# Kernel optimization log

Measured on AMD Instinct MI355X. Metric: run time of the kernel, lower is better.

## Reference

```python
import jax, jax.numpy as jnp
import numpy as np

N_NODES = 50000
D_IN = 128
D_OUT = 128
N_EDGES = 800000


def setup_inputs() -> dict:
    key = jax.random.key(0)
    ks = jax.random.split(key, 6)
    x = jax.random.normal(ks[0], (N_NODES, D_IN), dtype=jnp.float32)
    # xavier-uniform-ish init for the per-support weights
    limit = float(np.sqrt(6.0 / (D_IN + D_OUT)))
    weights = jax.random.uniform(ks[1], (2, D_IN, D_OUT), dtype=jnp.float32,
                                 minval=-limit, maxval=limit)
    edge_idx0 = jax.random.randint(ks[2], (2, N_EDGES), 0, N_NODES, dtype=jnp.int64 if jax.config.jax_enable_x64 else jnp.int32)
    vals0 = jax.random.uniform(ks[3], (N_EDGES,), dtype=jnp.float32)
    edge_idx1 = jax.random.randint(ks[4], (2, N_EDGES), 0, N_NODES, dtype=jnp.int64 if jax.config.jax_enable_x64 else jnp.int32)
    vals1 = jax.random.uniform(ks[5], (N_EDGES,), dtype=jnp.float32)
    return {"x": x, "weights": weights, "edge_idx0": edge_idx0, "vals0": vals0,
            "edge_idx1": edge_idx1, "vals1": vals1}


def _spmm(edge_idx, vals, dense, n_rows):
    # (sparse COO A) @ dense : out[row] += vals * dense[col]
    rows, cols = edge_idx[0], edge_idx[1]
    gathered = dense[cols] * vals[:, None]  # [E, D_OUT]
    return jax.ops.segment_sum(gathered, rows, num_segments=n_rows)


def reference(x, weights, edge_idx0, vals0, edge_idx1, vals1):
    n = x.shape[0]
    out = jnp.zeros((n, D_OUT), dtype=x.dtype)
    for w, ei, v in ((weights[0], edge_idx0, vals0), (weights[1], edge_idx1, vals1)):
        pre_sup = x @ w                       # [N, D_OUT] dense GEMM
        out = out + _spmm(ei, v, pre_sup, n)  # SpMM accumulate
    return jax.nn.relu(out)
```

## Files before the change

kernel.cpp:

```cpp
#include <hip/hip_runtime.h>

#define N_NODES 50000
#define D 128
#define N_EDGES 800000
#define SCAN_BLOCKS ((N_NODES + 255) / 256)
#define GEMM_BLOCKS ((N_NODES + 63) / 64)
#define BINS 196
#define NB1 256
#define CH1 3125
#define P2_CAP 9472

typedef __attribute__((ext_vector_type(8))) short short8;
typedef __attribute__((ext_vector_type(4))) float f32x4;

__device__ __forceinline__ unsigned short f2bf(float f) {
    unsigned u = __builtin_bit_cast(unsigned, f);
    u += 0x7FFFu + ((u >> 16) & 1u);
    return (unsigned short)(u >> 16);
}
__device__ __forceinline__ float bflo(unsigned p) {
    return __builtin_bit_cast(float, p << 16);
}
__device__ __forceinline__ float bfhi(unsigned p) {
    return __builtin_bit_cast(float, p & 0xFFFF0000u);
}

__global__ __launch_bounds__(256) void wt_build(const float* __restrict__ w,
                                                unsigned short* __restrict__ wt) {
    int i = blockIdx.x * 256 + threadIdx.x;
    if (i < 2 * D * D) {
        int s = i >> 14, rem = i & 16383, c = rem >> 7, k = rem & 127;
        wt[i] = f2bf(w[s * D * D + k * D + c]);
    }
}

template<int NS>
__device__ __forceinline__ void gemm_body(const float* __restrict__ x,
                                          const unsigned short* __restrict__ wt,
                                          unsigned short* __restrict__ pre0,
                                          unsigned short* __restrict__ pre1,
                                          int n_rows, int blk) {
    const int lane = threadIdx.x & 63;
    const int wid  = threadIdx.x >> 6;
    const int q    = lane >> 4;
    const int rlo  = lane & 15;
    const int r0   = blk * 64 + wid * 16;
    if (r0 >= n_rows) return;

    const float4* x4 = (const float4*)x;
    int arow  = r0 + rlo;
    int arowc = arow < n_rows ? arow : n_rows - 1;

    short8 afr[4];
    #pragma unroll
    for (int kb = 0; kb < 4; ++kb) {
        float4 fa = x4[(size_t)arowc * 32 + kb * 8 + q * 2];
        float4 fb = x4[(size_t)arowc * 32 + kb * 8 + q * 2 + 1];
        short8 a;
        a[0] = (short)f2bf(fa.x); a[1] = (short)f2bf(fa.y);
        a[2] = (short)f2bf(fa.z); a[3] = (short)f2bf(fa.w);
        a[4] = (short)f2bf(fb.x); a[5] = (short)f2bf(fb.y);
        a[6] = (short)f2bf(fb.z); a[7] = (short)f2bf(fb.w);
        afr[kb] = a;
    }

    const short8* wt8 = (const short8*)wt;
    f32x4 acc[NS][8];
    #pragma unroll
    for (int s = 0; s < NS; ++s)
        #pragma unroll
        for (int t = 0; t < 8; ++t)
            acc[s][t] = (f32x4){0.f, 0.f, 0.f, 0.f};

    #pragma unroll
    for (int t = 0; t < 8; ++t) {
        int c = t * 16 + rlo;
        #pragma unroll
        for (int kb = 0; kb < 4; ++kb) {
            short8 b0 = wt8[(size_t)c * 16 + kb * 4 + q];
            acc[0][t] = __builtin_amdgcn_mfma_f32_16x16x32_bf16(afr[kb], b0, acc[0][t], 0, 0, 0);
            if (NS == 2) {
                short8 b1 = wt8[(size_t)(D + c) * 16 + kb * 4 + q];
                acc[1][t] = __builtin_amdgcn_mfma_f32_16x16x32_bf16(afr[kb], b1, acc[1][t], 0, 0, 0);
            }
        }
    }

    #pragma unroll
    for (int i = 0; i < 4; ++i) {
        int rw = r0 + q * 4 + i;
        if (rw < n_rows) {
            #pragma unroll
            for (int t = 0; t < 8; ++t) {
                pre0[(size_t)rw * D + t * 16 + rlo] = f2bf(acc[0][t][i]);
                if (NS == 2) pre1[(size_t)rw * D + t * 16 + rlo] = f2bf(acc[1][t][i]);
            }
        }
    }
}


__global__ __launch_bounds__(256) void p1_count(const int* __restrict__ r0,
                                                const int* __restrict__ r1,
                                                int* __restrict__ h) {
    int s = blockIdx.y, blk = blockIdx.x;
    const int* r = s ? r1 : r0;
    __shared__ int hist[BINS];
    for (int i = threadIdx.x; i < BINS; i += 256) hist[i] = 0;
    __syncthreads();
    int start = blk * CH1, end = start + CH1;
    for (int e = start + (int)threadIdx.x; e < end; e += 256)
        atomicAdd(&hist[r[e] >> 8], 1);
    __syncthreads();
    for (int i = threadIdx.x; i < BINS; i += 256)
        h[(size_t)(s * NB1 + blk) * BINS + i] = hist[i];
}

__global__ __launch_bounds__(256) void binred(const int* __restrict__ h,
                                              int* __restrict__ bintot) {
    int s = blockIdx.y, bin = blockIdx.x, t = threadIdx.x;
    int v = h[(size_t)(s * NB1 + t) * BINS + bin];
    const int lane = t & 63, wid = t >> 6;
    __shared__ int ws[4];
    #pragma unroll
    for (int o = 32; o > 0; o >>= 1) v += __shfl_down(v, o);
    if (lane == 0) ws[wid] = v;
    __syncthreads();
    if (t == 0) bintot[s * BINS + bin] = ws[0] + ws[1] + ws[2] + ws[3];
}

__global__ __launch_bounds__(256) void binscan(const int* __restrict__ bintot,
                                               int* __restrict__ binbase) {
    int s = blockIdx.x, t = threadIdx.x;
    int v = (t < BINS) ? bintot[s * BINS + t] : 0;
    const int lane = t & 63, wid = t >> 6;
    __shared__ int ws[4];
    int incl = v;
    #pragma unroll
    for (int o = 1; o < 64; o <<= 1) { int tv = __shfl_up(incl, o); if (lane >= o) incl += tv; }
    if (lane == 63) ws[wid] = incl;
    __syncthreads();
    int wbase = 0;
    #pragma unroll
    for (int j = 0; j < 4; ++j) wbase += (j < wid) ? ws[j] : 0;
    int excl = wbase + incl - v;
    if (t < BINS) binbase[s * (BINS + 1) + t] = excl;
    if (t == BINS - 1) binbase[s * (BINS + 1) + BINS] = excl + v;
}

__global__ __launch_bounds__(256) void blkscan(int* __restrict__ h,
                                               const int* __restrict__ binbase) {
    int s = blockIdx.y, bin = blockIdx.x, t = threadIdx.x;
    size_t idx = (size_t)(s * NB1 + t) * BINS + bin;
    int v = h[idx];
    const int lane = t & 63, wid = t >> 6;
    __shared__ int ws[4];
    int incl = v;
    #pragma unroll
    for (int o = 1; o < 64; o <<= 1) { int tv = __shfl_up(incl, o); if (lane >= o) incl += tv; }
    if (lane == 63) ws[wid] = incl;
    __syncthreads();
    int wbase = 0;
    #pragma unroll
    for (int j = 0; j < 4; ++j) wbase += (j < wid) ? ws[j] : 0;
    h[idx] = binbase[s * (BINS + 1) + bin] + (wbase + incl - v);
}

__global__ __launch_bounds__(256) void k_fill_gemm(const float* __restrict__ x,
                                                   const unsigned short* __restrict__ wt,
                                                   unsigned short* __restrict__ pre0,
                                                   unsigned short* __restrict__ pre1,
                                                   const int* __restrict__ r0, const int* __restrict__ c0,
                                                   const float* __restrict__ v0,
                                                   const int* __restrict__ r1, const int* __restrict__ c1,
                                                   const float* __restrict__ v1,
                                                   const int* __restrict__ h,
                                                   int2* __restrict__ rec, int n_rows) {
    int bid = blockIdx.x;
    if (bid < 2 * NB1) {
        int s = bid & 1, blk = bid >> 1;
        const int*   r = s ? r1 : r0;
        const int*   c = s ? c1 : c0;
        const float* v = s ? v1 : v0;
        int2* rs = rec + (size_t)s * N_EDGES;
        __shared__ int base[BINS];
        __shared__ int cnt2[BINS];
        for (int i = threadIdx.x; i < BINS; i += 256) {
            base[i] = h[(size_t)(s * NB1 + blk) * BINS + i];
            cnt2[i] = 0;
        }
        __syncthreads();
        int start = blk * CH1, end = start + CH1;
        for (int e = start + (int)threadIdx.x; e < end; e += 256) {
            int rr = r[e], cc = c[e];
            float vv = v[e];
            int bin = rr >> 8;
            int lr = atomicAdd(&cnt2[bin], 1);
            rs[base[bin] + lr] = make_int2((cc << 8) | (rr & 255), __float_as_int(vv));
        }
    } else {
        gemm_body<2>(x, wt, pre0, pre1, n_rows, bid - 2 * NB1);
    }
}

__global__ __launch_bounds__(256) void p2_sort(const int* __restrict__ binbase,
                                               const int2* __restrict__ rec,
                                               int2* __restrict__ ep,
                                               int* __restrict__ off) {
    int s = blockIdx.y, bin = blockIdx.x, t = threadIdx.x;
    int bs  = binbase[s * (BINS + 1) + bin];
    int be  = binbase[s * (BINS + 1) + bin + 1];
    int cnt = be - bs;
    const int2* rs = rec + (size_t)s * N_EDGES;
    int2* es = ep + (size_t)s * N_EDGES;
    __shared__ int  lc[256];
    __shared__ int  cur[256];
    __shared__ int  ws[4];
    __shared__ int2 stage[P2_CAP];
    lc[t] = 0;
    __syncthreads();
    bool staged = (cnt <= P2_CAP);
    for (int i = t; i < cnt; i += 256) {
        int2 R = rs[bs + i];
        if (staged) stage[i] = R;
        atomicAdd(&lc[R.x & 255], 1);
    }
    __syncthreads();
    int v = lc[t];
    const int lane = t & 63, wid = t >> 6;
    int incl = v;
    #pragma unroll
    for (int o = 1; o < 64; o <<= 1) { int tv = __shfl_up(incl, o); if (lane >= o) incl += tv; }
    if (lane == 63) ws[wid] = incl;
    __syncthreads();
    int wbase = 0;
    #pragma unroll
    for (int j = 0; j < 4; ++j) wbase += (j < wid) ? ws[j] : 0;
    int excl = wbase + incl - v;
    int row = bin * 256 + t;
    if (row < N_NODES) off[s * (N_NODES + 1) + row] = bs + excl;
    if (bin == 0 && t == 0) off[s * (N_NODES + 1) + N_NODES] = N_EDGES;
    cur[t] = excl;
    __syncthreads();
    for (int i = t; i < cnt; i += 256) {
        int2 R = staged ? stage[i] : rs[bs + i];
        int p = atomicAdd(&cur[R.x & 255], 1);
        es[bs + p] = make_int2(R.x >> 8, R.y);
    }
}

__device__ __forceinline__ void row_acc(const int2* __restrict__ ep,
                                        const unsigned short* __restrict__ pre,
                                        int b, int e, int lane, float& ax, float& ay) {
    int i = b;
    for (; i + 7 < e; i += 8) {
        int2 E[8];
        unsigned P[8];
        #pragma unroll
        for (int j = 0; j < 8; ++j) E[j] = ep[i + j];
        #pragma unroll
        for (int j = 0; j < 8; ++j) P[j] = *(const unsigned*)(pre + (size_t)E[j].x * D + 2 * lane);
        #pragma unroll
        for (int j = 0; j < 8; ++j) {
            float w = __int_as_float(E[j].y);
            ax = fmaf(w, bflo(P[j]), ax);
            ay = fmaf(w, bfhi(P[j]), ay);
        }
    }
    if (i + 3 < e) {
        int2 E[4];
        unsigned P[4];
        #pragma unroll
        for (int j = 0; j < 4; ++j) E[j] = ep[i + j];
        #pragma unroll
        for (int j = 0; j < 4; ++j) P[j] = *(const unsigned*)(pre + (size_t)E[j].x * D + 2 * lane);
        #pragma unroll
        for (int j = 0; j < 4; ++j) {
            float w = __int_as_float(E[j].y);
            ax = fmaf(w, bflo(P[j]), ax);
            ay = fmaf(w, bfhi(P[j]), ay);
        }
        i += 4;
    }
    for (; i < e; ++i) {
        int2 e0 = ep[i];
        float w = __int_as_float(e0.y);
        unsigned p = *(const unsigned*)(pre + (size_t)e0.x * D + 2 * lane);
        ax = fmaf(w, bflo(p), ax);
        ay = fmaf(w, bfhi(p), ay);
    }
}

__global__ __launch_bounds__(256) void gather_fused(const int* __restrict__ off_base,
                                                    const int2* __restrict__ ep_base,
                                                    const unsigned short* __restrict__ pre0,
                                                    const unsigned short* __restrict__ pre1,
                                                    float* __restrict__ out, int n_rows) {
    const int lane = threadIdx.x & 63;
    const int wid  = threadIdx.x >> 6;
    const int wpg  = 4 * gridDim.x;
    const int2* ep1b = ep_base + N_EDGES;
    const int* o1 = off_base + (N_NODES + 1);
    float2* out2 = (float2*)out;
    for (int r = blockIdx.x * 4 + wid; r < n_rows; r += wpg) {
        float ax0 = 0.f, ay0 = 0.f, ax1 = 0.f, ay1 = 0.f;
        int i0 = off_base[r], e0 = off_base[r + 1];
        int i1 = o1[r],       e1 = o1[r + 1];
        while (i0 + 7 < e0 && i1 + 7 < e1) {
            int2 E0[8], E1[8];
            unsigned P0[8], P1[8];
            #pragma unroll
            for (int j = 0; j < 8; ++j) { E0[j] = ep_base[i0 + j]; E1[j] = ep1b[i1 + j]; }
            #pragma unroll
            for (int j = 0; j < 8; ++j) {
                P0[j] = *(const unsigned*)(pre0 + (size_t)E0[j].x * D + 2 * lane);
                P1[j] = *(const unsigned*)(pre1 + (size_t)E1[j].x * D + 2 * lane);
            }
            #pragma unroll
            for (int j = 0; j < 8; ++j) {
                float w0 = __int_as_float(E0[j].y);
                float w1 = __int_as_float(E1[j].y);
                ax0 = fmaf(w0, bflo(P0[j]), ax0);
                ay0 = fmaf(w0, bfhi(P0[j]), ay0);
                ax1 = fmaf(w1, bflo(P1[j]), ax1);
                ay1 = fmaf(w1, bfhi(P1[j]), ay1);
            }
            i0 += 8; i1 += 8;
        }
        row_acc(ep_base, pre0, i0, e0, lane, ax0, ay0);
        row_acc(ep1b,    pre1, i1, e1, lane, ax1, ay1);
        float2 o;
        o.x = fmaxf(ax0 + ax1, 0.f);
        o.y = fmaxf(ay0 + ay1, 0.f);
        out2[(size_t)r * 64 + lane] = o;
    }
}

__global__ __launch_bounds__(256) void gemm_mfma2(const float* __restrict__ x,
                                                  const unsigned short* __restrict__ wt,
                                                  unsigned short* __restrict__ pre0,
                                                  unsigned short* __restrict__ pre1, int n_rows) {
    gemm_body<2>(x, wt, pre0, pre1, n_rows, blockIdx.x);
}
__global__ __launch_bounds__(256) void gemm_mfma1(const float* __restrict__ x,
                                                  const unsigned short* __restrict__ wt,
                                                  unsigned short* __restrict__ pre, int n_rows) {
    gemm_body<1>(x, wt, pre, pre, n_rows, blockIdx.x);
}

__global__ __launch_bounds__(256) void hist_rank(const int* __restrict__ r0,
                                                 const int* __restrict__ r1,
                                                 int* __restrict__ cnt_base,
                                                 int* __restrict__ rank_base, int n_edges) {
    int s = blockIdx.y;
    const int* r = s ? r1 : r0;
    int* cnt  = cnt_base + s * N_NODES;
    int* rank = rank_base + (size_t)s * N_EDGES;
    for (int e = blockIdx.x * 256 + threadIdx.x; e < n_edges; e += gridDim.x * 256)
        rank[e] = atomicAdd(&cnt[r[e]], 1);
}

__global__ __launch_bounds__(256) void scanA(const int* __restrict__ cnt_base,
                                             int* __restrict__ bsum) {
    int s = blockIdx.y;
    int i = blockIdx.x * 256 + threadIdx.x;
    int v = (i < N_NODES) ? cnt_base[s * N_NODES + i] : 0;
    const int lane = threadIdx.x & 63;
    const int wid  = threadIdx.x >> 6;
    __shared__ int ws[4];
    #pragma unroll
    for (int off = 32; off > 0; off >>= 1) v += __shfl_down(v, off);
    if (lane == 0) ws[wid] = v;
    __syncthreads();
    if (threadIdx.x == 0)
        bsum[s * SCAN_BLOCKS + blockIdx.x] = ws[0] + ws[1] + ws[2] + ws[3];
}

__global__ __launch_bounds__(256) void scanC2(const int* __restrict__ cnt_base,
                                              const int* __restrict__ bsum,
                                              int* __restrict__ off_base) {
    int s = blockIdx.y;
    int t = threadIdx.x;
    const int lane = t & 63;
    const int wid  = t >> 6;
    __shared__ int ws[4];
    __shared__ int base_s;
    int bv = (t < (int)blockIdx.x && t < SCAN_BLOCKS) ? bsum[s * SCAN_BLOCKS + t] : 0;
    #pragma unroll
    for (int off = 32; off > 0; off >>= 1) bv += __shfl_down(bv, off);
    if (lane == 0) ws[wid] = bv;
    __syncthreads();
    if (t == 0) base_s = ws[0] + ws[1] + ws[2] + ws[3];
    __syncthreads();
    int base = base_s;
    __syncthreads();
    int i = blockIdx.x * 256 + t;
    int v = (i < N_NODES) ? cnt_base[s * N_NODES + i] : 0;
    int incl = v;
    #pragma unroll
    for (int off = 1; off < 64; off <<= 1) {
        int tv = __shfl_up(incl, off);
        if (lane >= off) incl += tv;
    }
    if (lane == 63) ws[wid] = incl;
    __syncthreads();
    int wbase = 0;
    #pragma unroll
    for (int j = 0; j < 4; ++j) wbase += (j < wid) ? ws[j] : 0;
    int* off = off_base + s * (N_NODES + 1);
    if (i < N_NODES)
        off[i] = base + wbase + incl - v;
    if (blockIdx.x == 0 && t == 0)
        off[N_NODES] = N_EDGES;
}

__global__ __launch_bounds__(256) void scatter_csr(const int* __restrict__ r0, const int* __restrict__ c0,
                                                   const float* __restrict__ v0,
                                                   const int* __restrict__ r1, const int* __restrict__ c1,
                                                   const float* __restrict__ v1,
                                                   const int* __restrict__ off_base,
                                                   const int* __restrict__ rank_base,
                                                   int2* __restrict__ ep_base, int n_edges) {
    int s = blockIdx.y;
    const int*   r    = s ? r1 : r0;
    const int*   c    = s ? c1 : c0;
    const float* v    = s ? v1 : v0;
    const int*   off  = off_base + s * (N_NODES + 1);
    const int*   rank = rank_base + (size_t)s * N_EDGES;
    int2* ep = ep_base + (size_t)s * N_EDGES;
    for (int e = blockIdx.x * 256 + threadIdx.x; e < n_edges; e += gridDim.x * 256) {
        int p = off[r[e]] + rank[e];
        int2 rec;
        rec.x = c[e];
        rec.y = __float_as_int(v[e]);
        ep[p] = rec;
    }
}

template<int ACCUM_RELU>
__global__ __launch_bounds__(256) void gather_one(const int* __restrict__ off,
                                                  const int2* __restrict__ ep,
                                                  const unsigned short* __restrict__ pre,
                                                  float* __restrict__ out, int n_rows) {
    const int lane = threadIdx.x & 63;
    const int wid  = threadIdx.x >> 6;
    const int wpg  = 4 * gridDim.x;
    float2* out2 = (float2*)out;
    for (int r = blockIdx.x * 4 + wid; r < n_rows; r += wpg) {
        float ax = 0.f, ay = 0.f;
        row_acc(ep, pre, off[r], off[r + 1], lane, ax, ay);
        float2 o;
        if (ACCUM_RELU) {
            float2 prev = out2[(size_t)r * 64 + lane];
            o.x = fmaxf(prev.x + ax, 0.f);
            o.y = fmaxf(prev.y + ay, 0.f);
        } else {
            o.x = ax; o.y = ay;
        }
        out2[(size_t)r * 64 + lane] = o;
    }
}

extern "C" void kernel_launch(void* const* d_in, const int* in_sizes, int n_in,
                              void* d_out, int out_size, void* d_ws, size_t ws_size,
                              hipStream_t stream) {
    const float* x       = (const float*)d_in[0];
    const float* weights = (const float*)d_in[1];
    const int*   ei0     = (const int*)d_in[2];
    const float* v0      = (const float*)d_in[3];
    const int*   ei1     = (const int*)d_in[4];
    const float* v1      = (const float*)d_in[5];
    float* out = (float*)d_out;

    dim3 blk(256);
    const size_t PRE_B = (size_t)N_NODES * D * sizeof(unsigned short);
    const size_t WT_B  = (size_t)2 * D * D * sizeof(unsigned short);
    const size_t H_B   = (size_t)2 * NB1 * BINS * 4;
    const size_t BT_B  = (size_t)2 * BINS * 4;
    const size_t BB_B  = (size_t)2 * (BINS + 1) * 4;
    const size_t OFF_B = (size_t)2 * (N_NODES + 1) * 4;
    const size_t E8    = (size_t)2 * N_EDGES * sizeof(int2);

    char* wsb = (char*)d_ws;
    size_t needNew = 2 * PRE_B + WT_B + H_B + BT_B + BB_B + OFF_B + 2 * E8;
    size_t needA1 = 2 * PRE_B + WT_B
                  + (size_t)(2 * (N_NODES + 1) + 2 * N_NODES + 2 * SCAN_BLOCKS) * 4
                  + E8 + (size_t)2 * N_EDGES * 4;

    if (ws_size >= needNew) {
        unsigned short* pre0 = (unsigned short*)wsb;
        unsigned short* pre1 = (unsigned short*)(wsb + PRE_B);
        unsigned short* wt   = (unsigned short*)(wsb + 2 * PRE_B);
        int*  h       = (int*)(wsb + 2 * PRE_B + WT_B);
        int*  bintot  = (int*)((char*)h + H_B);
        int*  binbase = (int*)((char*)bintot + BT_B);
        int*  off     = (int*)((char*)binbase + BB_B);
        int2* rec     = (int2*)((char*)off + OFF_B);
        int2* ep      = rec + (size_t)2 * N_EDGES;

        wt_build<<<128, blk, 0, stream>>>(weights, wt);
        p1_count<<<dim3(NB1, 2), blk, 0, stream>>>(ei0, ei1, h);
        binred  <<<dim3(BINS, 2), blk, 0, stream>>>(h, bintot);
        binscan <<<2, blk, 0, stream>>>(bintot, binbase);
        blkscan <<<dim3(BINS, 2), blk, 0, stream>>>(h, binbase);
        k_fill_gemm<<<2 * NB1 + GEMM_BLOCKS, blk, 0, stream>>>(
            x, wt, pre0, pre1,
            ei0, ei0 + N_EDGES, v0, ei1, ei1 + N_EDGES, v1,
            h, rec, N_NODES);
        p2_sort<<<dim3(BINS, 2), blk, 0, stream>>>(binbase, rec, ep, off);
        gather_fused<<<12500, blk, 0, stream>>>(off, ep, pre0, pre1, out, N_NODES);
    } else if (ws_size >= needA1) {
        unsigned short* pre0 = (unsigned short*)wsb;
        unsigned short* pre1 = (unsigned short*)(wsb + PRE_B);
        unsigned short* wt   = (unsigned short*)(wsb + 2 * PRE_B);
        int*  off  = (int*)(wsb + 2 * PRE_B + WT_B);
        int*  cnt  = off + 2 * (N_NODES + 1);
        int*  bsum = cnt + 2 * N_NODES;
        int2* ep   = (int2*)(bsum + 2 * SCAN_BLOCKS);
        int*  rank = (int*)(ep + (size_t)2 * N_EDGES);

        hipMemsetAsync(cnt, 0, (size_t)2 * N_NODES * sizeof(int), stream);
        wt_build<<<128, blk, 0, stream>>>(weights, wt);
        hist_rank<<<dim3(1024, 2), blk, 0, stream>>>(ei0, ei1, cnt, rank, N_EDGES);
        gemm_mfma2<<<GEMM_BLOCKS, blk, 0, stream>>>(x, wt, pre0, pre1, N_NODES);
        scanA<<<dim3(SCAN_BLOCKS, 2), blk, 0, stream>>>(cnt, bsum);
        scanC2<<<dim3(SCAN_BLOCKS, 2), blk, 0, stream>>>(cnt, bsum, off);
        scatter_csr<<<dim3(1024, 2), blk, 0, stream>>>(ei0, ei0 + N_EDGES, v0,
                                                       ei1, ei1 + N_EDGES, v1,
                                                       off, rank, ep, N_EDGES);
        gather_fused<<<12500, blk, 0, stream>>>(off, ep, pre0, pre1, out, N_NODES);
    } else {
        unsigned short* pre = (unsigned short*)wsb;
        unsigned short* wt  = (unsigned short*)(wsb + PRE_B);
        int*  off  = (int*)(wsb + PRE_B + WT_B);
        int*  cnt  = off + (N_NODES + 1);
        int*  bsum = cnt + N_NODES;
        int2* ep   = (int2*)(bsum + SCAN_BLOCKS);
        int*  rank = (int*)pre;

        wt_build<<<128, blk, 0, stream>>>(weights, wt);
        const int* rows[2] = {ei0, ei1};
        const int* cols[2] = {ei0 + N_EDGES, ei1 + N_EDGES};
        const float* vals[2] = {v0, v1};
        for (int s = 0; s < 2; ++s) {
            hipMemsetAsync(cnt, 0, (size_t)N_NODES * sizeof(int), stream);
            hist_rank<<<dim3(1024, 1), blk, 0, stream>>>(rows[s], rows[s], cnt, rank, N_EDGES);
            scanA<<<dim3(SCAN_BLOCKS, 1), blk, 0, stream>>>(cnt, bsum);
            scanC2<<<dim3(SCAN_BLOCKS, 1), blk, 0, stream>>>(cnt, bsum, off);
            scatter_csr<<<dim3(1024, 1), blk, 0, stream>>>(rows[s], cols[s], vals[s],
                                                           rows[s], cols[s], vals[s],
                                                           off, rank, ep, N_EDGES);
            gemm_mfma1<<<GEMM_BLOCKS, blk, 0, stream>>>(x, wt + (size_t)s * D * D, pre, N_NODES);
            if (s == 0)
                gather_one<0><<<12500, blk, 0, stream>>>(off, ep, pre, out, N_NODES);
            else
                gather_one<1><<<12500, blk, 0, stream>>>(off, ep, pre, out, N_NODES);
        }
    }
}
```

Measured before the change: 147.8 us.

## Process two rows per wave in gather and widen p2_sort to 512 threads

The gather kernel now has each wave handle rows r and r+N/2 together across both supports, giving four independent edge streams with 4-deep unrolling instead of two streams with 8-deep unrolling, and it launches half as many blocks. The aim is more independent loads in flight per wave. p2_sort drops its large LDS staging buffer, re-reads records from global memory, and runs 512 threads per block for higher occupancy. The trade-offs are more global reads in the sort and more tail work when the four rows have unequal degrees.

```diff
diff --git a/kernel.cpp b/kernel.cpp
--- a/kernel.cpp
+++ b/kernel.cpp
@@ -8,7 +8,6 @@
 #define BINS 196
 #define NB1 256
 #define CH1 3125
-#define P2_CAP 9472
 
 typedef __attribute__((ext_vector_type(8))) short short8;
 typedef __attribute__((ext_vector_type(4))) float f32x4;
@@ -203,7 +202,7 @@
     }
 }
 
-__global__ __launch_bounds__(256) void p2_sort(const int* __restrict__ binbase,
+__global__ __launch_bounds__(512) void p2_sort(const int* __restrict__ binbase,
                                                const int2* __restrict__ rec,
                                                int2* __restrict__ ep,
                                                int* __restrict__ off) {
@@ -213,37 +212,37 @@
     int cnt = be - bs;
     const int2* rs = rec + (size_t)s * N_EDGES;
     int2* es = ep + (size_t)s * N_EDGES;
-    __shared__ int  lc[256];
-    __shared__ int  cur[256];
-    __shared__ int  ws[4];
-    __shared__ int2 stage[P2_CAP];
-    lc[t] = 0;
-    __syncthreads();
-    bool staged = (cnt <= P2_CAP);
-    for (int i = t; i < cnt; i += 256) {
+    __shared__ int lc[256];
+    __shared__ int cur[256];
+    __shared__ int ws[4];
+    if (t < 256) lc[t] = 0;
+    __syncthreads();
+    for (int i = t; i < cnt; i += 512)
+        atomicAdd(&lc[rs[bs + i].x & 255], 1);
+    __syncthreads();
+    const int lane = t & 63, wid = t >> 6;
+    int v = 0, incl = 0;
+    if (t < 256) {
+        v = lc[t];
+        incl = v;
+        #pragma unroll
+        for (int o = 1; o < 64; o <<= 1) { int tv = __shfl_up(incl, o); if (lane >= o) incl += tv; }
+        if (lane == 63) ws[wid] = incl;
+    }
+    __syncthreads();
+    if (t < 256) {
+        int wbase = 0;
+        #pragma unroll
+        for (int j = 0; j < 4; ++j) wbase += (j < wid) ? ws[j] : 0;
+        int excl = wbase + incl - v;
+        int row = bin * 256 + t;
+        if (row < N_NODES) off[s * (N_NODES + 1) + row] = bs + excl;
+        cur[t] = excl;
+    }
+    if (bin == 0 && t == 0) off[s * (N_NODES + 1) + N_NODES] = N_EDGES;
+    __syncthreads();
+    for (int i = t; i < cnt; i += 512) {
         int2 R = rs[bs + i];
-        if (staged) stage[i] = R;
-        atomicAdd(&lc[R.x & 255], 1);
-    }
-    __syncthreads();
-    int v = lc[t];
-    const int lane = t & 63, wid = t >> 6;
-    int incl = v;
-    #pragma unroll
-    for (int o = 1; o < 64; o <<= 1) { int tv = __shfl_up(incl, o); if (lane >= o) incl += tv; }
-    if (lane == 63) ws[wid] = incl;
-    __syncthreads();
-    int wbase = 0;
-    #pragma unroll
-    for (int j = 0; j < 4; ++j) wbase += (j < wid) ? ws[j] : 0;
-    int excl = wbase + incl - v;
-    int row = bin * 256 + t;
-    if (row < N_NODES) off[s * (N_NODES + 1) + row] = bs + excl;
-    if (bin == 0 && t == 0) off[s * (N_NODES + 1) + N_NODES] = N_EDGES;
-    cur[t] = excl;
-    __syncthreads();
-    for (int i = t; i < cnt; i += 256) {
-        int2 R = staged ? stage[i] : rs[bs + i];
         int p = atomicAdd(&cur[R.x & 255], 1);
         es[bs + p] = make_int2(R.x >> 8, R.y);
     }
@@ -253,20 +252,6 @@
                                         const unsigned short* __restrict__ pre,
                                         int b, int e, int lane, float& ax, float& ay) {
     int i = b;
-    for (; i + 7 < e; i += 8) {
-        int2 E[8];
-        unsigned P[8];
-        #pragma unroll
-        for (int j = 0; j < 8; ++j) E[j] = ep[i + j];
-        #pragma unroll
-        for (int j = 0; j < 8; ++j) P[j] = *(const unsigned*)(pre + (size_t)E[j].x * D + 2 * lane);
-        #pragma unroll
-        for (int j = 0; j < 8; ++j) {
-            float w = __int_as_float(E[j].y);
-            ax = fmaf(w, bflo(P[j]), ax);
-            ay = fmaf(w, bfhi(P[j]), ay);
-        }
-    }
     if (i + 3 < e) {
         int2 E[4];
         unsigned P[4];
@@ -291,48 +276,99 @@
     }
 }
 
-__global__ __launch_bounds__(256) void gather_fused(const int* __restrict__ off_base,
-                                                    const int2* __restrict__ ep_base,
-                                                    const unsigned short* __restrict__ pre0,
-                                                    const unsigned short* __restrict__ pre1,
-                                                    float* __restrict__ out, int n_rows) {
+__device__ __forceinline__ void pair_acc(const int2* __restrict__ ep0, const int2* __restrict__ ep1,
+                                         const unsigned short* __restrict__ pre0,
+                                         const unsigned short* __restrict__ pre1,
+                                         int& i0, int e0, int& i1, int e1, int lane,
+                                         float& ax0, float& ay0, float& ax1, float& ay1) {
+    while (i0 + 3 < e0 && i1 + 3 < e1) {
+        int2 E0[4], E1[4];
+        unsigned P0[4], P1[4];
+        #pragma unroll
+        for (int j = 0; j < 4; ++j) { E0[j] = ep0[i0 + j]; E1[j] = ep1[i1 + j]; }
+        #pragma unroll
+        for (int j = 0; j < 4; ++j) {
+            P0[j] = *(const unsigned*)(pre0 + (size_t)E0[j].x * D + 2 * lane);
+            P1[j] = *(const unsigned*)(pre1 + (size_t)E1[j].x * D + 2 * lane);
+        }
+        #pragma unroll
+        for (int j = 0; j < 4; ++j) {
+            float w0 = __int_as_float(E0[j].y);
+            float w1 = __int_as_float(E1[j].y);
+            ax0 = fmaf(w0, bflo(P0[j]), ax0);
+            ay0 = fmaf(w0, bfhi(P0[j]), ay0);
+            ax1 = fmaf(w1, bflo(P1[j]), ax1);
+            ay1 = fmaf(w1, bfhi(P1[j]), ay1);
+        }
+        i0 += 4; i1 += 4;
+    }
+}
+
+__global__ __launch_bounds__(256) void gather_fused2(const int* __restrict__ off_base,
+                                                     const int2* __restrict__ ep_base,
+                                                     const unsigned short* __restrict__ pre0,
+                                                     const unsigned short* __restrict__ pre1,
+                                                     float* __restrict__ out, int n_rows) {
     const int lane = threadIdx.x & 63;
     const int wid  = threadIdx.x >> 6;
     const int wpg  = 4 * gridDim.x;
     const int2* ep1b = ep_base + N_EDGES;
+    const int* o0 = off_base;
     const int* o1 = off_base + (N_NODES + 1);
     float2* out2 = (float2*)out;
-    for (int r = blockIdx.x * 4 + wid; r < n_rows; r += wpg) {
+    const int H = n_rows >> 1;
+
+    for (int r = blockIdx.x * 4 + wid; r < H; r += wpg) {
+        int r2 = r + H;
+        int i0 = o0[r],  e0 = o0[r + 1];
+        int i1 = o1[r],  e1 = o1[r + 1];
+        int i2 = o0[r2], e2 = o0[r2 + 1];
+        int i3 = o1[r2], e3 = o1[r2 + 1];
         float ax0 = 0.f, ay0 = 0.f, ax1 = 0.f, ay1 = 0.f;
-        int i0 = off_base[r], e0 = off_base[r + 1];
-        int i1 = o1[r],       e1 = o1[r + 1];
-        while (i0 + 7 < e0 && i1 + 7 < e1) {
-            int2 E0[8], E1[8];
-            unsigned P0[8], P1[8];
+        float ax2 = 0.f, ay2 = 0.f, ax3 = 0.f, ay3 = 0.f;
+
+        while (i0 + 3 < e0 && i1 + 3 < e1 && i2 + 3 < e2 && i3 + 3 < e3) {
+            int2 E0[4], E1[4], E2[4], E3[4];
+            unsigned P0[4], P1[4], P2[4], P3[4];
             #pragma unroll
-            for (int j = 0; j < 8; ++j) { E0[j] = ep_base[i0 + j]; E1[j] = ep1b[i1 + j]; }
+            for (int j = 0; j < 4; ++j) {
+                E0[j] = ep_base[i0 + j]; E1[j] = ep1b[i1 + j];
+                E2[j] = ep_base[i2 + j]; E3[j] = ep1b[i3 + j];
+            }
             #pragma unroll
-            for (int j = 0; j < 8; ++j) {
+            for (int j = 0; j < 4; ++j) {
                 P0[j] = *(const unsigned*)(pre0 + (size_t)E0[j].x * D + 2 * lane);
                 P1[j] = *(const unsigned*)(pre1 + (size_t)E1[j].x * D + 2 * lane);
+                P2[j] = *(const unsigned*)(pre0 + (size_t)E2[j].x * D + 2 * lane);
+                P3[j] = *(const unsigned*)(pre1 + (size_t)E3[j].x * D + 2 * lane);
             }
             #pragma unroll
-            for (int j = 0; j < 8; ++j) {
+            for (int j = 0; j < 4; ++j) {
                 float w0 = __int_as_float(E0[j].y);
                 float w1 = __int_as_float(E1[j].y);
-                ax0 = fmaf(w0, bflo(P0[j]), ax0);
-                ay0 = fmaf(w0, bfhi(P0[j]), ay0);
-                ax1 = fmaf(w1, bflo(P1[j]), ax1);
-                ay1 = fmaf(w1, bfhi(P1[j]), ay1);
+                float w2 = __int_as_float(E2[j].y);
+                float w3 = __int_as_float(E3[j].y);
+                ax0 = fmaf(w0, bflo(P0[j]), ax0); ay0 = fmaf(w0, bfhi(P0[j]), ay0);
+                ax1 = fmaf(w1, bflo(P1[j]), ax1); ay1 = fmaf(w1, bfhi(P1[j]), ay1);
+                ax2 = fmaf(w2, bflo(P2[j]), ax2); ay2 = fmaf(w2, bfhi(P2[j]), ay2);
+                ax3 = fmaf(w3, bflo(P3[j]), ax3); ay3 = fmaf(w3, bfhi(P3[j]), ay3);
             }
-            i0 += 8; i1 += 8;
-        }
+            i0 += 4; i1 += 4; i2 += 4; i3 += 4;
+        }
+        pair_acc(ep_base, ep1b, pre0, pre1, i0, e0, i1, e1, lane, ax0, ay0, ax1, ay1);
+        pair_acc(ep_base, ep1b, pre0, pre1, i2, e2, i3, e3, lane, ax2, ay2, ax3, ay3);
         row_acc(ep_base, pre0, i0, e0, lane, ax0, ay0);
         row_acc(ep1b,    pre1, i1, e1, lane, ax1, ay1);
-        float2 o;
-        o.x = fmaxf(ax0 + ax1, 0.f);
-        o.y = fmaxf(ay0 + ay1, 0.f);
-        out2[(size_t)r * 64 + lane] = o;
+        row_acc(ep_base, pre0, i2, e2, lane, ax2, ay2);
+        row_acc(ep1b,    pre1, i3, e3, lane, ax3, ay3);
+
+        float2 oA, oB;
+        oA.x = fmaxf(ax0 + ax1, 0.f);
+        oA.y = fmaxf(ay0 + ay1, 0.f);
+        oB.x = fmaxf(ax2 + ax3, 0.f);
+        oB.y = fmaxf(ay2 + ay3, 0.f);
+        out2[(size_t)r * 64 + lane]  = oA;
+        out2[(size_t)r2 * 64 + lane] = oB;
     }
 }
 
@@ -437,6 +473,31 @@
     }
 }
 
+__global__ __launch_bounds__(256) void gather_fused(const int* __restrict__ off_base,
+                                                    const int2* __restrict__ ep_base,
+                                                    const unsigned short* __restrict__ pre0,
+                                                    const unsigned short* __restrict__ pre1,
+                                                    float* __restrict__ out, int n_rows) {
+    const int lane = threadIdx.x & 63;
+    const int wid  = threadIdx.x >> 6;
+    const int wpg  = 4 * gridDim.x;
+    const int2* ep1b = ep_base + N_EDGES;
+    const int* o1 = off_base + (N_NODES + 1);
+    float2* out2 = (float2*)out;
+    for (int r = blockIdx.x * 4 + wid; r < n_rows; r += wpg) {
+        float ax0 = 0.f, ay0 = 0.f, ax1 = 0.f, ay1 = 0.f;
+        int i0 = off_base[r], e0 = off_base[r + 1];
+        int i1 = o1[r],       e1 = o1[r + 1];
+        pair_acc(ep_base, ep1b, pre0, pre1, i0, e0, i1, e1, lane, ax0, ay0, ax1, ay1);
+        row_acc(ep_base, pre0, i0, e0, lane, ax0, ay0);
+        row_acc(ep1b,    pre1, i1, e1, lane, ax1, ay1);
+        float2 o;
+        o.x = fmaxf(ax0 + ax1, 0.f);
+        o.y = fmaxf(ay0 + ay1, 0.f);
+        out2[(size_t)r * 64 + lane] = o;
+    }
+}
+
 template<int ACCUM_RELU>
 __global__ __launch_bounds__(256) void gather_one(const int* __restrict__ off,
                                                   const int2* __restrict__ ep,
@@ -507,8 +568,8 @@
             x, wt, pre0, pre1,
             ei0, ei0 + N_EDGES, v0, ei1, ei1 + N_EDGES, v1,
             h, rec, N_NODES);
-        p2_sort<<<dim3(BINS, 2), blk, 0, stream>>>(binbase, rec, ep, off);
-        gather_fused<<<12500, blk, 0, stream>>>(off, ep, pre0, pre1, out, N_NODES);
+        p2_sort<<<dim3(BINS, 2), dim3(512), 0, stream>>>(binbase, rec, ep, off);
+        gather_fused2<<<6250, blk, 0, stream>>>(off, ep, pre0, pre1, out, N_NODES);
     } else if (ws_size >= needA1) {
         unsigned short* pre0 = (unsigned short*)wsb;
         unsigned short* pre1 = (unsigned short*)(wsb + PRE_B);
```

Result: slower. 162.9 us (+10.2%).
